# Performance work log

Measured on AMD Instinct MI355X. Metric: run time of the kernel, lower is better.

## Reference

```python
import jax, jax.numpy as jnp
import numpy as np

L, R, H = 4, 4, 16          # left heads, right heads, per-head hidden
D = L * H                    # 64 = left*h = right*h = output_size
B, T = 2, 96


def setup_inputs() -> dict:
    key = jax.random.key(0)
    ks = jax.random.split(key, 16)
    p = lambda k, s: jax.random.normal(k, s, dtype=jnp.float32) * 0.1
    return {
        "queries": jax.random.normal(ks[0], (B, T, D, D), dtype=jnp.float32),
        "keys":    jax.random.normal(ks[1], (B, T, D, D), dtype=jnp.float32),
        "values":  jax.random.normal(ks[2], (B, T, D, D), dtype=jnp.float32),
        "Wq_row": p(ks[3], (D, D)), "Wq_col": p(ks[4], (D, D)), "bq": p(ks[5], (D, D)),
        "Wk_row": p(ks[6], (D, D)), "Wk_col": p(ks[7], (D, D)), "bk": p(ks[8], (D, D)),
        "Wv_row": p(ks[9], (D, D)), "Wv_col": p(ks[10], (D, D)), "bv": p(ks[11], (D, D)),
        "Wo_row": p(ks[12], (D, D)), "Wo_col": p(ks[13], (D, D)), "bo": p(ks[14], (D, D)),
    }


def _pdense(x, Wr, Wc, b):
    # PartialDenseLayer: dense transform on BOTH trailing axes of the 2D token
    # [..., i, j] -> [..., a, b]
    return jnp.einsum('...ij,ia,jb->...ab', x, Wr, Wc) + b


def _separate(x):
    # [B, T, L*H, R*H] -> [B, T, L, R, H, H]
    b, t = x.shape[:2]
    return x.reshape(b, t, L, H, R, H).transpose(0, 1, 2, 4, 3, 5)


def _merge(x):
    # [B, T, L, R, H, H] -> [B, T, L*H, R*H]
    b, t = x.shape[:2]
    return x.transpose(0, 1, 2, 4, 3, 5).reshape(b, t, L * H, R * H)


def reference(queries, keys, values,
              Wq_row, Wq_col, bq, Wk_row, Wk_col, bk,
              Wv_row, Wv_col, bv, Wo_row, Wo_col, bo):
    h = float(H)
    q = _separate(_pdense(queries, Wq_row, Wq_col, bq) / h)  # [B,Tq,L,R,H,H]
    k = _separate(_pdense(keys,    Wk_row, Wk_col, bk) / h)  # [B,Tk,L,R,H,H]
    v = _separate(_pdense(values,  Wv_row, Wv_col, bv) / h)  # [B,Tk,L,R,H,H]
    # similarity_method (method_one): q @ k^T on trailing HxH matrices
    logits = jnp.einsum('bilrpm,bjlrqm->bijlrpq', q, k) / h  # [B,Tq,Tk,L,R,H,H]
    w = jax.nn.softmax(logits, axis=2)                        # softmax over key axis (-5)
    # causal ordering mask over the (L, R) head grid (band_part lower-tri)
    mask = jnp.tril(jnp.ones((L, R), dtype=w.dtype))
    w = w * mask[None, None, None, :, :, None, None]
    # merge_method (method_one): matmul with values then sum over keys
    out = jnp.einsum('bijlrpm,bjlrmq->bilrpq', w, v)          # [B,Tq,L,R,H,H]
    return _pdense(_merge(out), Wo_row, Wo_col, bo) / h       # [B,Tq,D,D]
```

## Files before the change

### kernel.cpp

```cpp
#include <hip/hip_runtime.h>
#include <hip/hip_bf16.h>
#include <math.h>

typedef unsigned int uint32;
typedef unsigned short ushort_t;
typedef __attribute__((ext_vector_type(8))) short s8v;
typedef __attribute__((ext_vector_type(16))) float f16v;
typedef __attribute__((ext_vector_type(2))) unsigned int u2v;

#define LH 4
#define RH 4
#define DD 64
#define BB 2
#define TT 96
#define NTOK (BB*TT)
#define HEADS 16
#define VHEADS 10
#define INV_H 0.0625f
#define LOG2E 1.4426950408889634f
#define QKV_BLOCKS 288
#define ZF_BLOCKS 48

struct U4 { uint32 x, y, z, w; };

__device__ __forceinline__ uint32 f2bf(float f) {
    return (uint32)__builtin_bit_cast(ushort_t, __float2bfloat16(f));
}
__device__ __forceinline__ uint32 pkbf(float lo, float hi) {
    return f2bf(lo) | (f2bf(hi) << 16);
}
__device__ __forceinline__ float bf2f(uint32 u) {
    return __uint_as_float(u << 16);
}
__device__ __forceinline__ void hl_pair(float v0, float v1, uint32 &hw, uint32 &lw) {
    uint32 h0 = f2bf(v0), h1 = f2bf(v1);
    hw = h0 | (h1 << 16);
    lw = pkbf(v0 - bf2f(h0), v1 - bf2f(h1));
}
__device__ __forceinline__ void hswap(uint32 &a, uint32 &b, int h) {
#if __has_builtin(__builtin_amdgcn_permlane32_swap)
    u2v rr = __builtin_amdgcn_permlane32_swap(a, b, false, false);
    a = rr.x; b = rr.y;
#else
    uint32 xa = (uint32)__shfl_xor((int)a, 32, 64);
    uint32 xb = (uint32)__shfl_xor((int)b, 32, 64);
    uint32 na = (h == 0) ? xb : a;
    uint32 nb = (h == 0) ? b  : xa;
    a = na; b = nb;
#endif
}

__global__ __launch_bounds__(256) void pdense_qkv_mfma(
    const float* __restrict__ Xq, const float* __restrict__ Xk, const float* __restrict__ Xv,
    const float* __restrict__ Wq_row, const float* __restrict__ Wq_col, const float* __restrict__ bq,
    const float* __restrict__ Wk_row, const float* __restrict__ Wk_col, const float* __restrict__ bk,
    const float* __restrict__ Wv_row, const float* __restrict__ Wv_col, const float* __restrict__ bv,
    ushort_t* __restrict__ q_bf, ushort_t* __restrict__ k_bf,
    ushort_t* __restrict__ vt_bf, float* __restrict__ att)
{
    __shared__ float lds_t1[4][32][68];

    const int bid = blockIdx.x;
    if (bid >= QKV_BLOCKS) {
        const int zb = bid - QKV_BLOCKS;
        float4* a4 = (float4*)att;
        #pragma unroll
        for (int it = 0; it < 16; ++it)
            a4[(size_t)zb * 4096 + it * 256 + threadIdx.x] = float4{0.f, 0.f, 0.f, 0.f};
        return;
    }
    const int wv = threadIdx.x >> 6;
    const int task = bid * 4 + wv;
    const int proj = task / (NTOK * 2);
    const int rem  = task % (NTOK * 2);
    const int token = rem >> 1;
    const int ch = rem & 1;
    const int lane = threadIdx.x & 63;
    const int c5 = lane & 31, h = lane >> 5;
    const int c = ch * 32 + c5;
    const int bI = token / TT, t = token % TT;

    const float* X  = (proj == 0) ? Xq : (proj == 1) ? Xk : Xv;
    const float* Wc = (proj == 0) ? Wq_col : (proj == 1) ? Wk_col : Wv_col;
    const float* Wr = (proj == 0) ? Wq_row : (proj == 1) ? Wk_row : Wv_row;
    const float* bs = (proj == 0) ? bq : (proj == 1) ? bk : bv;
    const float* Xp = X + (size_t)token * 4096;
    const float scale = (proj == 0) ? (INV_H * INV_H * LOG2E) : INV_H;

    const f16v fz = {0,0,0,0,0,0,0,0,0,0,0,0,0,0,0,0};

    f16v t1_0 = fz, t1_1 = fz;
    #pragma unroll
    for (int n = 0; n < 4; ++n) {
        const int k0 = n * 16 + 8 * h;
        U4 ub = { pkbf(Wc[(k0 + 0) * 64 + c], Wc[(k0 + 1) * 64 + c]),
                  pkbf(Wc[(k0 + 2) * 64 + c], Wc[(k0 + 3) * 64 + c]),
                  pkbf(Wc[(k0 + 4) * 64 + c], Wc[(k0 + 5) * 64 + c]),
                  pkbf(Wc[(k0 + 6) * 64 + c], Wc[(k0 + 7) * 64 + c]) };
        s8v bf = __builtin_bit_cast(s8v, ub);
        {
            const float* xr = Xp + (size_t)c5 * 64 + k0;
            float4 xa = *(const float4*)xr, xb = *(const float4*)(xr + 4);
            U4 u = { pkbf(xa.x, xa.y), pkbf(xa.z, xa.w), pkbf(xb.x, xb.y), pkbf(xb.z, xb.w) };
            t1_0 = __builtin_amdgcn_mfma_f32_32x32x16_bf16(__builtin_bit_cast(s8v, u), bf, t1_0, 0, 0, 0);
        }
        {
            const float* xr = Xp + (size_t)(32 + c5) * 64 + k0;
            float4 xa = *(const float4*)xr, xb = *(const float4*)(xr + 4);
            U4 u = { pkbf(xa.x, xa.y), pkbf(xa.z, xa.w), pkbf(xb.x, xb.y), pkbf(xb.z, xb.w) };
            t1_1 = __builtin_amdgcn_mfma_f32_32x32x16_bf16(__builtin_bit_cast(s8v, u), bf, t1_1, 0, 0, 0);
        }
    }

    #pragma unroll
    for (int tt = 0; tt < 16; ++tt) {
        const int i = (tt & 3) + 8 * (tt >> 2) + 4 * h;
        lds_t1[wv][c5][i]      = t1_0[tt];
        lds_t1[wv][c5][32 + i] = t1_1[tt];
    }
    __syncthreads();

    s8v bfr[4];
    #pragma unroll
    for (int n = 0; n < 4; ++n) {
        const float* p = &lds_t1[wv][c5][n * 16 + 8 * h];
        float4 xa = *(const float4*)p, xb = *(const float4*)(p + 4);
        U4 u = { pkbf(xa.x, xa.y), pkbf(xa.z, xa.w), pkbf(xb.x, xb.y), pkbf(xb.z, xb.w) };
        bfr[n] = __builtin_bit_cast(s8v, u);
    }

    #pragma unroll
    for (int At = 0; At < 2; ++At) {
        const int a0 = 32 * At + c5;
        f16v y = fz;
        #pragma unroll
        for (int n = 0; n < 4; ++n) {
            const int k0 = n * 16 + 8 * h;
            U4 ua = { pkbf(Wr[(k0 + 0) * 64 + a0], Wr[(k0 + 1) * 64 + a0]),
                      pkbf(Wr[(k0 + 2) * 64 + a0], Wr[(k0 + 3) * 64 + a0]),
                      pkbf(Wr[(k0 + 4) * 64 + a0], Wr[(k0 + 5) * 64 + a0]),
                      pkbf(Wr[(k0 + 6) * 64 + a0], Wr[(k0 + 7) * 64 + a0]) };
            y = __builtin_amdgcn_mfma_f32_32x32x16_bf16(
                    __builtin_bit_cast(s8v, ua), bfr[n], y, 0, 0, 0);
        }
        #pragma unroll
        for (int rg = 0; rg < 4; ++rg) {
            #pragma unroll
            for (int e = 0; e < 4; ++e) {
                const int a = 32 * At + 8 * rg + 4 * h + e;
                const float val = (y[rg * 4 + e] + bs[a * 64 + c]) * scale;
                const ushort_t ov = (ushort_t)f2bf(val);
                const size_t base =
                    ((size_t)((bI * HEADS + (a >> 4) * RH + (c >> 4)) * TT + t)) * 256;
                if (proj == 0)      q_bf[base + (a & 15) * 16 + (c & 15)] = ov;
                else if (proj == 1) k_bf[base + (a & 15) * 16 + (c & 15)] = ov;
                else                vt_bf[base + (c & 15) * 16 + (a & 15)] = ov;
            }
        }
    }
}

__global__ __launch_bounds__(256) void pdense_out_mfma2(
    const float* __restrict__ att,
    const float* __restrict__ Wo_row, const float* __restrict__ Wo_col,
    const float* __restrict__ bo, float* __restrict__ out)
{
    __shared__ float lds_t1[4][32][68];

    const int wv = threadIdx.x >> 6;
    const int task = blockIdx.x * 4 + wv;
    const int token = task >> 1, ch = task & 1;
    const int lane = threadIdx.x & 63;
    const int c5 = lane & 31, h = lane >> 5;
    const int c = ch * 32 + c5;

    const float* Xp = att + (size_t)token * 4096;
    const f16v fz = {0,0,0,0,0,0,0,0,0,0,0,0,0,0,0,0};

    f16v t1_0 = fz, t1_1 = fz;
    #pragma unroll
    for (int n = 0; n < 4; ++n) {
        const int k0 = n * 16 + 8 * h;
        uint32 bh0, bl0, bh1, bl1, bh2, bl2, bh3, bl3;
        hl_pair(Wo_col[(k0 + 0) * 64 + c], Wo_col[(k0 + 1) * 64 + c], bh0, bl0);
        hl_pair(Wo_col[(k0 + 2) * 64 + c], Wo_col[(k0 + 3) * 64 + c], bh1, bl1);
        hl_pair(Wo_col[(k0 + 4) * 64 + c], Wo_col[(k0 + 5) * 64 + c], bh2, bl2);
        hl_pair(Wo_col[(k0 + 6) * 64 + c], Wo_col[(k0 + 7) * 64 + c], bh3, bl3);
        U4 ubh = {bh0, bh1, bh2, bh3}, ubl = {bl0, bl1, bl2, bl3};
        s8v bh = __builtin_bit_cast(s8v, ubh), bl = __builtin_bit_cast(s8v, ubl);
        #pragma unroll
        for (int T = 0; T < 2; ++T) {
            const float* xr = Xp + (size_t)(32 * T + c5) * 64 + k0;
            float4 xa = *(const float4*)xr, xb = *(const float4*)(xr + 4);
            uint32 hw0, lw0, hw1, lw1, hw2, lw2, hw3, lw3;
            hl_pair(xa.x, xa.y, hw0, lw0);
            hl_pair(xa.z, xa.w, hw1, lw1);
            hl_pair(xb.x, xb.y, hw2, lw2);
            hl_pair(xb.z, xb.w, hw3, lw3);
            U4 uh = {hw0, hw1, hw2, hw3}, ul = {lw0, lw1, lw2, lw3};
            s8v ah = __builtin_bit_cast(s8v, uh), al = __builtin_bit_cast(s8v, ul);
            f16v acc = (T == 0) ? t1_0 : t1_1;
            acc = __builtin_amdgcn_mfma_f32_32x32x16_bf16(ah, bh, acc, 0, 0, 0);
            acc = __builtin_amdgcn_mfma_f32_32x32x16_bf16(al, bh, acc, 0, 0, 0);
            acc = __builtin_amdgcn_mfma_f32_32x32x16_bf16(ah, bl, acc, 0, 0, 0);
            if (T == 0) t1_0 = acc; else t1_1 = acc;
        }
    }

    #pragma unroll
    for (int tt = 0; tt < 16; ++tt) {
        const int i = (tt & 3) + 8 * (tt >> 2) + 4 * h;
        lds_t1[wv][c5][i]      = t1_0[tt];
        lds_t1[wv][c5][32 + i] = t1_1[tt];
    }
    __syncthreads();

    s8v bfh[4], bfl[4];
    #pragma unroll
    for (int n = 0; n < 4; ++n) {
        const float* p = &lds_t1[wv][c5][n * 16 + 8 * h];
        float4 xa = *(const float4*)p, xb = *(const float4*)(p + 4);
        uint32 h0, l0, h1, l1, h2, l2, h3, l3;
        hl_pair(xa.x, xa.y, h0, l0);
        hl_pair(xa.z, xa.w, h1, l1);
        hl_pair(xb.x, xb.y, h2, l2);
        hl_pair(xb.z, xb.w, h3, l3);
        U4 uh = {h0, h1, h2, h3}, ul = {l0, l1, l2, l3};
        bfh[n] = __builtin_bit_cast(s8v, uh);
        bfl[n] = __builtin_bit_cast(s8v, ul);
    }

    #pragma unroll
    for (int At = 0; At < 2; ++At) {
        const int a0 = 32 * At + c5;
        f16v y = fz;
        #pragma unroll
        for (int n = 0; n < 4; ++n) {
            const int k0 = n * 16 + 8 * h;
            uint32 ah0, al0, ah1, al1, ah2, al2, ah3, al3;
            hl_pair(Wo_row[(k0 + 0) * 64 + a0], Wo_row[(k0 + 1) * 64 + a0], ah0, al0);
            hl_pair(Wo_row[(k0 + 2) * 64 + a0], Wo_row[(k0 + 3) * 64 + a0], ah1, al1);
            hl_pair(Wo_row[(k0 + 4) * 64 + a0], Wo_row[(k0 + 5) * 64 + a0], ah2, al2);
            hl_pair(Wo_row[(k0 + 6) * 64 + a0], Wo_row[(k0 + 7) * 64 + a0], ah3, al3);
            U4 uah = {ah0, ah1, ah2, ah3}, ual = {al0, al1, al2, al3};
            s8v awh = __builtin_bit_cast(s8v, uah), awl = __builtin_bit_cast(s8v, ual);
            y = __builtin_amdgcn_mfma_f32_32x32x16_bf16(awh, bfh[n], y, 0, 0, 0);
            y = __builtin_amdgcn_mfma_f32_32x32x16_bf16(awh, bfl[n], y, 0, 0, 0);
            y = __builtin_amdgcn_mfma_f32_32x32x16_bf16(awl, bfh[n], y, 0, 0, 0);
        }
        #pragma unroll
        for (int rg = 0; rg < 4; ++rg) {
            #pragma unroll
            for (int e = 0; e < 4; ++e) {
                const int a = 32 * At + 8 * rg + 4 * h + e;
                out[(size_t)token * 4096 + a * 64 + c] =
                    (y[rg * 4 + e] + bo[a * 64 + c]) * INV_H;
            }
        }
    }
}

__global__ __launch_bounds__(256, 4) void attn_kernel(
    const ushort_t* __restrict__ q_bf,
    const ushort_t* __restrict__ k_bf,
    const ushort_t* __restrict__ vt_bf,
    float* __restrict__ att)
{
    __shared__ float lds_z[4][64][9];
    __shared__ float lds_pv[4][64][17];

    const int ip = blockIdx.x % (TT / 2);
    const int vh = (blockIdx.x / (TT / 2)) % VHEADS;
    const int bI = blockIdx.x / ((TT / 2) * VHEADS);
    const int l = (vh >= 1) + (vh >= 3) + (vh >= 6);
    const int r = vh - (l * (l + 1)) / 2;
    const int head = l * RH + r;
    const int i0 = ip * 2;
    const int lane = threadIdx.x & 63;
    const int wv = threadIdx.x >> 6;
    const int c5 = lane & 31;
    const int h  = lane >> 5;

    const size_t hb = (size_t)(bI * HEADS + head) * TT * 256;
    const int frow = (c5 & 15) * 16 + 8 * h;

    s8v qf = *(const s8v*)(q_bf + hb + (size_t)(i0 + (c5 >> 4)) * 256 + frow);
    const ushort_t* kb = k_bf + hb + frow;
    const ushort_t* vb = vt_bf + hb + frow;

    const int jb = wv * (TT / 4);
    const f16v fz16 = {0,0,0,0,0,0,0,0,0,0,0,0,0,0,0,0};

    float ls[8] = {0,0,0,0,0,0,0,0};
    #pragma unroll 3
    for (int jp = 0; jp < 12; ++jp) {
        const int j0g = jb + jp * 2;
        s8v kf = *(const s8v*)(kb + (size_t)(j0g + (c5 >> 4)) * 256);
        f16v d = __builtin_amdgcn_mfma_f32_32x32x16_bf16(kf, qf, fz16, 0, 0, 0);
        #pragma unroll
        for (int t = 0; t < 8; ++t)
            ls[t] += exp2f(d[t]) + exp2f(d[t + 8]);
    }
    #pragma unroll
    for (int t = 0; t < 8; ++t) lds_z[wv][lane][t] = ls[t];
    __syncthreads();
    float inv[8];
    #pragma unroll
    for (int t = 0; t < 8; ++t) {
        float s = lds_z[0][lane][t] + lds_z[1][lane][t]
                + lds_z[2][lane][t] + lds_z[3][lane][t];
        inv[t] = 1.f / s;
    }

    f16v pv = fz16;
    #pragma unroll 2
    for (int jp = 0; jp < 12; ++jp) {
        const int j0g = jb + jp * 2;
        s8v kf = *(const s8v*)(kb + (size_t)(j0g + (c5 >> 4)) * 256);
        f16v d = __builtin_amdgcn_mfma_f32_32x32x16_bf16(kf, qf, fz16, 0, 0, 0);
        float w[16];
        #pragma unroll
        for (int t = 0; t < 8; ++t) {
            w[t]     = exp2f(d[t])     * inv[t];
            w[t + 8] = exp2f(d[t + 8]) * inv[t];
        }
        uint32 A0 = pkbf(w[0],  w[1]),  A1 = pkbf(w[2],  w[3]);
        uint32 A2 = pkbf(w[4],  w[5]),  A3 = pkbf(w[6],  w[7]);
        uint32 B0 = pkbf(w[8],  w[9]),  B1 = pkbf(w[10], w[11]);
        uint32 B2 = pkbf(w[12], w[13]), B3 = pkbf(w[14], w[15]);
        hswap(A2, A0, h); hswap(A3, A1, h);
        hswap(B2, B0, h); hswap(B3, B1, h);
        U4 fa = {A0, A1, A2, A3};
        U4 fb = {B0, B1, B2, B3};
        s8v vf0 = *(const s8v*)(vb + (size_t)(j0g + 0) * 256);
        s8v vf1 = *(const s8v*)(vb + (size_t)(j0g + 1) * 256);
        pv = __builtin_amdgcn_mfma_f32_32x32x16_bf16(__builtin_bit_cast(s8v, fa), vf0, pv, 0, 0, 0);
        pv = __builtin_amdgcn_mfma_f32_32x32x16_bf16(__builtin_bit_cast(s8v, fb), vf1, pv, 0, 0, 0);
    }

    #pragma unroll
    for (int t = 0; t < 16; ++t) lds_pv[wv][lane][t] = pv[t];
    __syncthreads();

    if (c5 < 16) {
        #pragma unroll
        for (int rr = 0; rr < 4; ++rr) {
            const int reg = wv * 4 + rr;
            float v = lds_pv[0][lane][reg] + lds_pv[1][lane][reg]
                    + lds_pv[2][lane][reg] + lds_pv[3][lane][reg];
            const int row = rr + 8 * wv + 4 * h;
            const int i = row >> 4, p = row & 15;
            att[((size_t)(bI * TT + i0 + i) * DD + l * 16 + p) * DD + r * 16 + c5] = v;
        }
    }
}

extern "C" void kernel_launch(void* const* d_in, const int* in_sizes, int n_in,
                              void* d_out, int out_size, void* d_ws, size_t ws_size,
                              hipStream_t stream) {
    const float* queries = (const float*)d_in[0];
    const float* keys    = (const float*)d_in[1];
    const float* values  = (const float*)d_in[2];
    const float* Wq_row  = (const float*)d_in[3];
    const float* Wq_col  = (const float*)d_in[4];
    const float* bq      = (const float*)d_in[5];
    const float* Wk_row  = (const float*)d_in[6];
    const float* Wk_col  = (const float*)d_in[7];
    const float* bk      = (const float*)d_in[8];
    const float* Wv_row  = (const float*)d_in[9];
    const float* Wv_col  = (const float*)d_in[10];
    const float* bv      = (const float*)d_in[11];
    const float* Wo_row  = (const float*)d_in[12];
    const float* Wo_col  = (const float*)d_in[13];
    const float* bo      = (const float*)d_in[14];
    float* out = (float*)d_out;

    const size_t SEP = (size_t)BB * HEADS * TT * 256;
    ushort_t* q_bf  = (ushort_t*)d_ws;
    ushort_t* k_bf  = q_bf + SEP;
    ushort_t* vt_bf = k_bf + SEP;
    float*    att   = (float*)(vt_bf + SEP);

    pdense_qkv_mfma<<<QKV_BLOCKS + ZF_BLOCKS, 256, 0, stream>>>(
        queries, keys, values,
        Wq_row, Wq_col, bq, Wk_row, Wk_col, bk, Wv_row, Wv_col, bv,
        q_bf, k_bf, vt_bf, att);

    attn_kernel<<<BB * VHEADS * (TT / 2), 256, 0, stream>>>(q_bf, k_bf, vt_bf, att);

    pdense_out_mfma2<<<NTOK * 2 / 4, 256, 0, stream>>>(
        att, Wo_row, Wo_col, bo, out);
}
```

Before: 63.45 us.

## Fuse attention with output projection via LDS-resident attention tile

Merges the attention kernel and the output partial-dense kernel into one kernel. Each block handles two query tokens across all ten unmasked heads and writes the attention result into a zero-initialised shared-memory tile instead of global memory, then runs the output projection from LDS. This removes one launch, the global zero-fill of the attention buffer, and the global write and re-read of the intermediate. The cost is parallelism: only 96 blocks run, and each wave serially processes up to three heads over all 96 keys instead of 960 blocks splitting the keys four ways.

```diff
diff --git a/kernel.cpp b/kernel.cpp
--- a/kernel.cpp
+++ b/kernel.cpp
@@ -19,7 +19,6 @@
 #define INV_H 0.0625f
 #define LOG2E 1.4426950408889634f
 #define QKV_BLOCKS 288
-#define ZF_BLOCKS 48
 
 struct U4 { uint32 x, y, z, w; };
 
@@ -56,21 +55,12 @@
     const float* __restrict__ Wk_row, const float* __restrict__ Wk_col, const float* __restrict__ bk,
     const float* __restrict__ Wv_row, const float* __restrict__ Wv_col, const float* __restrict__ bv,
     ushort_t* __restrict__ q_bf, ushort_t* __restrict__ k_bf,
-    ushort_t* __restrict__ vt_bf, float* __restrict__ att)
+    ushort_t* __restrict__ vt_bf)
 {
     __shared__ float lds_t1[4][32][68];
 
-    const int bid = blockIdx.x;
-    if (bid >= QKV_BLOCKS) {
-        const int zb = bid - QKV_BLOCKS;
-        float4* a4 = (float4*)att;
-        #pragma unroll
-        for (int it = 0; it < 16; ++it)
-            a4[(size_t)zb * 4096 + it * 256 + threadIdx.x] = float4{0.f, 0.f, 0.f, 0.f};
-        return;
-    }
     const int wv = threadIdx.x >> 6;
-    const int task = bid * 4 + wv;
+    const int task = blockIdx.x * 4 + wv;
     const int proj = task / (NTOK * 2);
     const int rem  = task % (NTOK * 2);
     const int token = rem >> 1;
@@ -160,22 +150,93 @@
     }
 }
 
-__global__ __launch_bounds__(256) void pdense_out_mfma2(
-    const float* __restrict__ att,
+__global__ __launch_bounds__(256) void attn_out_fused(
+    const ushort_t* __restrict__ q_bf,
+    const ushort_t* __restrict__ k_bf,
+    const ushort_t* __restrict__ vt_bf,
     const float* __restrict__ Wo_row, const float* __restrict__ Wo_col,
     const float* __restrict__ bo, float* __restrict__ out)
 {
+    __shared__ float attS[2 * 64 * 68];
     __shared__ float lds_t1[4][32][68];
 
-    const int wv = threadIdx.x >> 6;
-    const int task = blockIdx.x * 4 + wv;
-    const int token = task >> 1, ch = task & 1;
-    const int lane = threadIdx.x & 63;
-    const int c5 = lane & 31, h = lane >> 5;
+    const int ip = blockIdx.x % (TT / 2);
+    const int bI = blockIdx.x / (TT / 2);
+    const int i0 = ip * 2;
+    const int tid = threadIdx.x;
+    const int wv = tid >> 6;
+    const int lane = tid & 63;
+    const int c5 = lane & 31;
+    const int h  = lane >> 5;
+    const f16v fz = {0,0,0,0,0,0,0,0,0,0,0,0,0,0,0,0};
+
+    for (int z = tid; z < 2 * 64 * 68; z += 256) attS[z] = 0.f;
+    __syncthreads();
+
+    const int frow = (c5 & 15) * 16 + 8 * h;
+    for (int vh = wv; vh < VHEADS; vh += 4) {
+        const int l = (vh >= 1) + (vh >= 3) + (vh >= 6);
+        const int r = vh - (l * (l + 1)) / 2;
+        const int head = l * RH + r;
+        const size_t hb = (size_t)(bI * HEADS + head) * TT * 256;
+
+        s8v qf = *(const s8v*)(q_bf + hb + (size_t)(i0 + (c5 >> 4)) * 256 + frow);
+        const ushort_t* kb = k_bf + hb + frow;
+        const ushort_t* vb = vt_bf + hb + frow;
+
+        float ls[8] = {0,0,0,0,0,0,0,0};
+        #pragma unroll 4
+        for (int jp = 0; jp < TT / 2; ++jp) {
+            const int j0g = jp * 2;
+            s8v kf = *(const s8v*)(kb + (size_t)(j0g + (c5 >> 4)) * 256);
+            f16v d = __builtin_amdgcn_mfma_f32_32x32x16_bf16(kf, qf, fz, 0, 0, 0);
+            #pragma unroll
+            for (int t = 0; t < 8; ++t)
+                ls[t] += exp2f(d[t]) + exp2f(d[t + 8]);
+        }
+        float inv[8];
+        #pragma unroll
+        for (int t = 0; t < 8; ++t) inv[t] = 1.f / ls[t];
+
+        f16v pv = fz;
+        #pragma unroll 2
+        for (int jp = 0; jp < TT / 2; ++jp) {
+            const int j0g = jp * 2;
+            s8v kf = *(const s8v*)(kb + (size_t)(j0g + (c5 >> 4)) * 256);
+            f16v d = __builtin_amdgcn_mfma_f32_32x32x16_bf16(kf, qf, fz, 0, 0, 0);
+            float w[16];
+            #pragma unroll
+            for (int t = 0; t < 8; ++t) {
+                w[t]     = exp2f(d[t])     * inv[t];
+                w[t + 8] = exp2f(d[t + 8]) * inv[t];
+            }
+            uint32 A0 = pkbf(w[0],  w[1]),  A1 = pkbf(w[2],  w[3]);
+            uint32 A2 = pkbf(w[4],  w[5]),  A3 = pkbf(w[6],  w[7]);
+            uint32 B0 = pkbf(w[8],  w[9]),  B1 = pkbf(w[10], w[11]);
+            uint32 B2 = pkbf(w[12], w[13]), B3 = pkbf(w[14], w[15]);
+            hswap(A2, A0, h); hswap(A3, A1, h);
+            hswap(B2, B0, h); hswap(B3, B1, h);
+            U4 fa = {A0, A1, A2, A3};
+            U4 fb = {B0, B1, B2, B3};
+            s8v vf0 = *(const s8v*)(vb + (size_t)(j0g + 0) * 256);
+            s8v vf1 = *(const s8v*)(vb + (size_t)(j0g + 1) * 256);
+            pv = __builtin_amdgcn_mfma_f32_32x32x16_bf16(__builtin_bit_cast(s8v, fa), vf0, pv, 0, 0, 0);
+            pv = __builtin_amdgcn_mfma_f32_32x32x16_bf16(__builtin_bit_cast(s8v, fb), vf1, pv, 0, 0, 0);
+        }
+
+        if (c5 < 16) {
+            #pragma unroll
+            for (int reg = 0; reg < 16; ++reg) {
+                const int row = (reg & 3) + 8 * (reg >> 2) + 4 * h;
+                const int i = row >> 4, p = row & 15;
+                attS[((i * 64) + l * 16 + p) * 68 + r * 16 + c5] = pv[reg];
+            }
+        }
+    }
+    __syncthreads();
+
+    const int tok = wv >> 1, ch = wv & 1;
     const int c = ch * 32 + c5;
-
-    const float* Xp = att + (size_t)token * 4096;
-    const f16v fz = {0,0,0,0,0,0,0,0,0,0,0,0,0,0,0,0};
 
     f16v t1_0 = fz, t1_1 = fz;
     #pragma unroll
@@ -190,7 +251,7 @@
         s8v bh = __builtin_bit_cast(s8v, ubh), bl = __builtin_bit_cast(s8v, ubl);
         #pragma unroll
         for (int T = 0; T < 2; ++T) {
-            const float* xr = Xp + (size_t)(32 * T + c5) * 64 + k0;
+            const float* xr = &attS[((tok * 64) + 32 * T + c5) * 68 + k0];
             float4 xa = *(const float4*)xr, xb = *(const float4*)(xr + 4);
             uint32 hw0, lw0, hw1, lw1, hw2, lw2, hw3, lw3;
             hl_pair(xa.x, xa.y, hw0, lw0);
@@ -253,104 +314,9 @@
             #pragma unroll
             for (int e = 0; e < 4; ++e) {
                 const int a = 32 * At + 8 * rg + 4 * h + e;
-                out[(size_t)token * 4096 + a * 64 + c] =
+                out[(size_t)(bI * TT + i0 + tok) * 4096 + a * 64 + c] =
                     (y[rg * 4 + e] + bo[a * 64 + c]) * INV_H;
             }
-        }
-    }
-}
-
-__global__ __launch_bounds__(256, 4) void attn_kernel(
-    const ushort_t* __restrict__ q_bf,
-    const ushort_t* __restrict__ k_bf,
-    const ushort_t* __restrict__ vt_bf,
-    float* __restrict__ att)
-{
-    __shared__ float lds_z[4][64][9];
-    __shared__ float lds_pv[4][64][17];
-
-    const int ip = blockIdx.x % (TT / 2);
-    const int vh = (blockIdx.x / (TT / 2)) % VHEADS;
-    const int bI = blockIdx.x / ((TT / 2) * VHEADS);
-    const int l = (vh >= 1) + (vh >= 3) + (vh >= 6);
-    const int r = vh - (l * (l + 1)) / 2;
-    const int head = l * RH + r;
-    const int i0 = ip * 2;
-    const int lane = threadIdx.x & 63;
-    const int wv = threadIdx.x >> 6;
-    const int c5 = lane & 31;
-    const int h  = lane >> 5;
-
-    const size_t hb = (size_t)(bI * HEADS + head) * TT * 256;
-    const int frow = (c5 & 15) * 16 + 8 * h;
-
-    s8v qf = *(const s8v*)(q_bf + hb + (size_t)(i0 + (c5 >> 4)) * 256 + frow);
-    const ushort_t* kb = k_bf + hb + frow;
-    const ushort_t* vb = vt_bf + hb + frow;
-
-    const int jb = wv * (TT / 4);
-    const f16v fz16 = {0,0,0,0,0,0,0,0,0,0,0,0,0,0,0,0};
-
-    float ls[8] = {0,0,0,0,0,0,0,0};
-    #pragma unroll 3
-    for (int jp = 0; jp < 12; ++jp) {
-        const int j0g = jb + jp * 2;
-        s8v kf = *(const s8v*)(kb + (size_t)(j0g + (c5 >> 4)) * 256);
-        f16v d = __builtin_amdgcn_mfma_f32_32x32x16_bf16(kf, qf, fz16, 0, 0, 0);
-        #pragma unroll
-        for (int t = 0; t < 8; ++t)
-            ls[t] += exp2f(d[t]) + exp2f(d[t + 8]);
-    }
-    #pragma unroll
-    for (int t = 0; t < 8; ++t) lds_z[wv][lane][t] = ls[t];
-    __syncthreads();
-    float inv[8];
-    #pragma unroll
-    for (int t = 0; t < 8; ++t) {
-        float s = lds_z[0][lane][t] + lds_z[1][lane][t]
-                + lds_z[2][lane][t] + lds_z[3][lane][t];
-        inv[t] = 1.f / s;
-    }
-
-    f16v pv = fz16;
-    #pragma unroll 2
-    for (int jp = 0; jp < 12; ++jp) {
-        const int j0g = jb + jp * 2;
-        s8v kf = *(const s8v*)(kb + (size_t)(j0g + (c5 >> 4)) * 256);
-        f16v d = __builtin_amdgcn_mfma_f32_32x32x16_bf16(kf, qf, fz16, 0, 0, 0);
-        float w[16];
-        #pragma unroll
-        for (int t = 0; t < 8; ++t) {
-            w[t]     = exp2f(d[t])     * inv[t];
-            w[t + 8] = exp2f(d[t + 8]) * inv[t];
-        }
-        uint32 A0 = pkbf(w[0],  w[1]),  A1 = pkbf(w[2],  w[3]);
-        uint32 A2 = pkbf(w[4],  w[5]),  A3 = pkbf(w[6],  w[7]);
-        uint32 B0 = pkbf(w[8],  w[9]),  B1 = pkbf(w[10], w[11]);
-        uint32 B2 = pkbf(w[12], w[13]), B3 = pkbf(w[14], w[15]);
-        hswap(A2, A0, h); hswap(A3, A1, h);
-        hswap(B2, B0, h); hswap(B3, B1, h);
-        U4 fa = {A0, A1, A2, A3};
-        U4 fb = {B0, B1, B2, B3};
-        s8v vf0 = *(const s8v*)(vb + (size_t)(j0g + 0) * 256);
-        s8v vf1 = *(const s8v*)(vb + (size_t)(j0g + 1) * 256);
-        pv = __builtin_amdgcn_mfma_f32_32x32x16_bf16(__builtin_bit_cast(s8v, fa), vf0, pv, 0, 0, 0);
-        pv = __builtin_amdgcn_mfma_f32_32x32x16_bf16(__builtin_bit_cast(s8v, fb), vf1, pv, 0, 0, 0);
-    }
-
-    #pragma unroll
-    for (int t = 0; t < 16; ++t) lds_pv[wv][lane][t] = pv[t];
-    __syncthreads();
-
-    if (c5 < 16) {
-        #pragma unroll
-        for (int rr = 0; rr < 4; ++rr) {
-            const int reg = wv * 4 + rr;
-            float v = lds_pv[0][lane][reg] + lds_pv[1][lane][reg]
-                    + lds_pv[2][lane][reg] + lds_pv[3][lane][reg];
-            const int row = rr + 8 * wv + 4 * h;
-            const int i = row >> 4, p = row & 15;
-            att[((size_t)(bI * TT + i0 + i) * DD + l * 16 + p) * DD + r * 16 + c5] = v;
         }
     }
 }
@@ -379,15 +345,12 @@
     ushort_t* q_bf  = (ushort_t*)d_ws;
     ushort_t* k_bf  = q_bf + SEP;
     ushort_t* vt_bf = k_bf + SEP;
-    float*    att   = (float*)(vt_bf + SEP);
-
-    pdense_qkv_mfma<<<QKV_BLOCKS + ZF_BLOCKS, 256, 0, stream>>>(
+
+    pdense_qkv_mfma<<<QKV_BLOCKS, 256, 0, stream>>>(
         queries, keys, values,
         Wq_row, Wq_col, bq, Wk_row, Wk_col, bk, Wv_row, Wv_col, bv,
-        q_bf, k_bf, vt_bf, att);
-
-    attn_kernel<<<BB * VHEADS * (TT / 2), 256, 0, stream>>>(q_bf, k_bf, vt_bf, att);
-
-    pdense_out_mfma2<<<NTOK * 2 / 4, 256, 0, stream>>>(
-        att, Wo_row, Wo_col, bo, out);
-}
+        q_bf, k_bf, vt_bf);
+
+    attn_out_fused<<<BB * (TT / 2), 256, 0, stream>>>(
+        q_bf, k_bf, vt_bf, Wo_row, Wo_col, bo, out);
+}
```

After: 133.4 us. +110.2%, slower.

## Use one-wave blocks for dense projections and split zero-fill into own kernel

Applied to the files above, without the earlier changes.

The QKV and output partial-dense kernels now launch one 64-thread block per task instead of packing four waves per 256-thread block. This gives the scheduler more, smaller blocks to spread across CUs, and each block needs less LDS. The zero-fill of the attention accumulator moves out of the QKV kernel into a separate launch. That removes the divergent zero-fill branch but adds an extra kernel launch.

```diff
diff --git a/kernel.cpp b/kernel.cpp
--- a/kernel.cpp
+++ b/kernel.cpp
@@ -18,8 +18,6 @@
 #define VHEADS 10
 #define INV_H 0.0625f
 #define LOG2E 1.4426950408889634f
-#define QKV_BLOCKS 288
-#define ZF_BLOCKS 48
 
 struct U4 { uint32 x, y, z, w; };
 
@@ -50,32 +48,22 @@
 #endif
 }
 
-__global__ __launch_bounds__(256) void pdense_qkv_mfma(
+__global__ __launch_bounds__(64) void pdense_qkv_mfma(
     const float* __restrict__ Xq, const float* __restrict__ Xk, const float* __restrict__ Xv,
     const float* __restrict__ Wq_row, const float* __restrict__ Wq_col, const float* __restrict__ bq,
     const float* __restrict__ Wk_row, const float* __restrict__ Wk_col, const float* __restrict__ bk,
     const float* __restrict__ Wv_row, const float* __restrict__ Wv_col, const float* __restrict__ bv,
     ushort_t* __restrict__ q_bf, ushort_t* __restrict__ k_bf,
-    ushort_t* __restrict__ vt_bf, float* __restrict__ att)
+    ushort_t* __restrict__ vt_bf)
 {
-    __shared__ float lds_t1[4][32][68];
-
-    const int bid = blockIdx.x;
-    if (bid >= QKV_BLOCKS) {
-        const int zb = bid - QKV_BLOCKS;
-        float4* a4 = (float4*)att;
-        #pragma unroll
-        for (int it = 0; it < 16; ++it)
-            a4[(size_t)zb * 4096 + it * 256 + threadIdx.x] = float4{0.f, 0.f, 0.f, 0.f};
-        return;
-    }
-    const int wv = threadIdx.x >> 6;
-    const int task = bid * 4 + wv;
+    __shared__ float lds_t1[32][68];
+
+    const int task = blockIdx.x;
     const int proj = task / (NTOK * 2);
     const int rem  = task % (NTOK * 2);
     const int token = rem >> 1;
     const int ch = rem & 1;
-    const int lane = threadIdx.x & 63;
+    const int lane = threadIdx.x;
     const int c5 = lane & 31, h = lane >> 5;
     const int c = ch * 32 + c5;
     const int bI = token / TT, t = token % TT;
@@ -115,15 +103,15 @@
     #pragma unroll
     for (int tt = 0; tt < 16; ++tt) {
         const int i = (tt & 3) + 8 * (tt >> 2) + 4 * h;
-        lds_t1[wv][c5][i]      = t1_0[tt];
-        lds_t1[wv][c5][32 + i] = t1_1[tt];
+        lds_t1[c5][i]      = t1_0[tt];
+        lds_t1[c5][32 + i] = t1_1[tt];
     }
     __syncthreads();
 
     s8v bfr[4];
     #pragma unroll
     for (int n = 0; n < 4; ++n) {
-        const float* p = &lds_t1[wv][c5][n * 16 + 8 * h];
+        const float* p = &lds_t1[c5][n * 16 + 8 * h];
         float4 xa = *(const float4*)p, xb = *(const float4*)(p + 4);
         U4 u = { pkbf(xa.x, xa.y), pkbf(xa.z, xa.w), pkbf(xb.x, xb.y), pkbf(xb.z, xb.w) };
         bfr[n] = __builtin_bit_cast(s8v, u);
@@ -160,17 +148,16 @@
     }
 }
 
-__global__ __launch_bounds__(256) void pdense_out_mfma2(
+__global__ __launch_bounds__(64) void pdense_out_mfma2(
     const float* __restrict__ att,
     const float* __restrict__ Wo_row, const float* __restrict__ Wo_col,
     const float* __restrict__ bo, float* __restrict__ out)
 {
-    __shared__ float lds_t1[4][32][68];
-
-    const int wv = threadIdx.x >> 6;
-    const int task = blockIdx.x * 4 + wv;
+    __shared__ float lds_t1[32][68];
+
+    const int task = blockIdx.x;
     const int token = task >> 1, ch = task & 1;
-    const int lane = threadIdx.x & 63;
+    const int lane = threadIdx.x;
     const int c5 = lane & 31, h = lane >> 5;
     const int c = ch * 32 + c5;
 
@@ -210,15 +197,15 @@
     #pragma unroll
     for (int tt = 0; tt < 16; ++tt) {
         const int i = (tt & 3) + 8 * (tt >> 2) + 4 * h;
-        lds_t1[wv][c5][i]      = t1_0[tt];
-        lds_t1[wv][c5][32 + i] = t1_1[tt];
+        lds_t1[c5][i]      = t1_0[tt];
+        lds_t1[c5][32 + i] = t1_1[tt];
     }
     __syncthreads();
 
     s8v bfh[4], bfl[4];
     #pragma unroll
     for (int n = 0; n < 4; ++n) {
-        const float* p = &lds_t1[wv][c5][n * 16 + 8 * h];
+        const float* p = &lds_t1[c5][n * 16 + 8 * h];
         float4 xa = *(const float4*)p, xb = *(const float4*)(p + 4);
         uint32 h0, l0, h1, l1, h2, l2, h3, l3;
         hl_pair(xa.x, xa.y, h0, l0);
@@ -258,6 +245,14 @@
             }
         }
     }
+}
+
+__global__ __launch_bounds__(256) void zerofill_att(float4* __restrict__ att4)
+{
+    #pragma unroll
+    for (int k2 = 0; k2 < 16; ++k2)
+        att4[(size_t)blockIdx.x * 4096 + k2 * 256 + threadIdx.x] =
+            float4{0.f, 0.f, 0.f, 0.f};
 }
 
 __global__ __launch_bounds__(256, 4) void attn_kernel(
@@ -381,13 +376,15 @@
     ushort_t* vt_bf = k_bf + SEP;
     float*    att   = (float*)(vt_bf + SEP);
 
-    pdense_qkv_mfma<<<QKV_BLOCKS + ZF_BLOCKS, 256, 0, stream>>>(
+    zerofill_att<<<48, 256, 0, stream>>>((float4*)att);
+
+    pdense_qkv_mfma<<<3 * NTOK * 2, 64, 0, stream>>>(
         queries, keys, values,
         Wq_row, Wq_col, bq, Wk_row, Wk_col, bk, Wv_row, Wv_col, bv,
-        q_bf, k_bf, vt_bf, att);
+        q_bf, k_bf, vt_bf);
 
     attn_kernel<<<BB * VHEADS * (TT / 2), 256, 0, stream>>>(q_bf, k_bf, vt_bf, att);
 
-    pdense_out_mfma2<<<NTOK * 2 / 4, 256, 0, stream>>>(
+    pdense_out_mfma2<<<NTOK * 2, 64, 0, stream>>>(
         att, Wo_row, Wo_col, bo, out);
 }
```

Measured after the change: 61.27 us. -3.4%, faster.
